# Kernel tuning notes

Hardware: AMD Instinct MI355X
Metric: run time of the kernel (lower is better)

The kernel has to match this reference:

```python
import jax, jax.numpy as jnp
import numpy as np
import math

B, T, D_MODEL, N_HEADS, K_CONV = 2, 2048, 2048, 16, 4
HEAD_DIM = D_MODEL // N_HEADS
EPS_GN = 1e-5


def setup_inputs() -> dict:
    key = jax.random.key(0)
    ks = jax.random.split(key, 16)
    s = 0.02
    # gamma bias init per reset_parameters (decays 0.9..0.9999 per head)
    min_d, max_d = 0.9, 0.9999
    tgt = 1.0 - np.exp(np.linspace(math.log(1 - min_d), math.log(1 - max_d), N_HEADS))
    gamma_bias = np.log(tgt / (1 - tgt)).astype(np.float32)
    return {
        "x": jax.random.normal(ks[0], (B, T, D_MODEL), jnp.float32),
        "Wq": jax.random.normal(ks[1], (D_MODEL, D_MODEL), jnp.float32) * s,
        "Wk": jax.random.normal(ks[2], (D_MODEL, D_MODEL), jnp.float32) * s,
        "Wv": jax.random.normal(ks[3], (D_MODEL, D_MODEL), jnp.float32) * s,
        "Wo": jax.random.normal(ks[4], (D_MODEL, D_MODEL), jnp.float32) * s,
        "conv_w": jax.random.normal(ks[5], (D_MODEL, K_CONV), jnp.float32) * 0.1,
        "conv_b": jnp.zeros((D_MODEL,), jnp.float32),
        "Wig": jax.random.normal(ks[6], (D_MODEL, D_MODEL), jnp.float32) * s,
        "b_ig": jnp.zeros((D_MODEL,), jnp.float32),
        "Wog": jax.random.normal(ks[7], (D_MODEL, D_MODEL), jnp.float32) * s,
        "b_og": jnp.zeros((D_MODEL,), jnp.float32),
        "Wg": jnp.zeros((N_HEADS, D_MODEL), jnp.float32),
        "b_g": jnp.asarray(gamma_bias),
        "gn_w": jnp.ones((D_MODEL,), jnp.float32),
        "gn_b": jnp.zeros((D_MODEL,), jnp.float32),
        "mn_w": jnp.ones((D_MODEL,), jnp.float32),
        "mn_b": jnp.zeros((D_MODEL,), jnp.float32),
    }


def _group_norm(x2d, w, b, groups, eps):
    # x2d: [N, C], normalize per group of C//groups channels
    N, C = x2d.shape
    xg = x2d.reshape(N, groups, C // groups)
    mu = xg.mean(-1, keepdims=True)
    var = ((xg - mu) ** 2).mean(-1, keepdims=True)
    xn = ((xg - mu) * jax.lax.rsqrt(var + eps)).reshape(N, C)
    return xn * w + b


def _causal_depthwise_conv(x, w, b):
    # x: [B,T,C], w: [C,K], b: [C] -> [B,T,C] causal depthwise conv + silu
    xt = jnp.transpose(x, (0, 2, 1))  # [B,C,T]
    xp = jnp.pad(xt, ((0, 0), (0, 0), (K_CONV - 1, 0)))
    y = jax.lax.conv_general_dilated(
        xp, w[:, None, :], (1,), "VALID",
        feature_group_count=D_MODEL,
        dimension_numbers=("NCH", "OIH", "NCH"))
    y = y + b[None, :, None]
    return jax.nn.silu(jnp.transpose(y, (0, 2, 1)))


def _l2norm(t):
    n = jnp.sqrt(jnp.sum(t * t, axis=-1, keepdims=True))
    return t / jnp.maximum(n, 1e-12)


def reference(x, Wq, Wk, Wv, Wo, conv_w, conv_b, Wig, b_ig, Wog, b_og, Wg, b_g, gn_w, gn_b, mn_w, mn_b):
    Bq, Tq, C = x.shape
    x_conv = _causal_depthwise_conv(x, conv_w, conv_b)  # [B,T,C]

    q = _l2norm((x @ Wq.T).reshape(Bq, Tq, N_HEADS, HEAD_DIM))
    k = _l2norm((x @ Wk.T).reshape(Bq, Tq, N_HEADS, HEAD_DIM))
    v = (x @ Wv.T).reshape(Bq, Tq, N_HEADS, HEAD_DIM)

    input_gate = jax.nn.sigmoid(x_conv @ Wig.T + b_ig).reshape(Bq, Tq, N_HEADS, HEAD_DIM)
    gamma = jax.nn.sigmoid(x_conv @ Wg.T + b_g).reshape(Bq, Tq, N_HEADS, 1)

    # gated elementwise linear recurrence: h_t = gamma_t * h_{t-1} + i_t * (k_t * v_t)
    bterm = input_gate * k * v                       # [B,T,H,D]
    aterm = jnp.broadcast_to(gamma, bterm.shape)     # [B,T,H,D]

    def scan_op(c1, c2):
        a1, b1 = c1
        a2, b2 = c2
        return (a1 * a2, a2 * b1 + b2)

    _, mem = jax.lax.associative_scan(scan_op, (aterm, bterm), axis=1)
    next_rnn_state = mem[:, -1]

    mem_n = _group_norm(mem.reshape(Bq * Tq, D_MODEL), mn_w, mn_b, N_HEADS, EPS_GN)
    mem_n = mem_n.reshape(Bq, Tq, N_HEADS, HEAD_DIM)

    out = (mem_n * q).reshape(Bq * Tq, C)
    out = _group_norm(out, gn_w, gn_b, N_HEADS, EPS_GN).reshape(Bq, Tq, C)

    output_gate = jax.nn.sigmoid(x_conv @ Wog.T + b_og)
    out = (out * output_gate) @ Wo.T

    new_conv_cache = jnp.transpose(x, (0, 2, 1))[:, :, -(K_CONV - 1):]
    return out, next_rnn_state, new_conv_cache
```

## Files before the change

kernel.cpp:

```cpp
#include <hip/hip_runtime.h>
#include <math.h>

#define B_ 2
#define T_ 2048
#define D_ 2048
#define H_ 16
#define M_ 4096
#define TD_ (T_ * D_)
#define EPS_ 1e-5f
#define NC_ 32
#define CL_ 64

typedef __bf16 bf16x8 __attribute__((ext_vector_type(8)));
typedef float f32x4 __attribute__((ext_vector_type(4)));

__device__ __forceinline__ float sigm(float z) { return 1.f / (1.f + __expf(-z)); }

__device__ __forceinline__ ushort f2bf(float f) {
    union { float f; uint u; } x; x.f = f;
    uint r = x.u + 0x7fffu + ((x.u >> 16) & 1u);
    return (ushort)(r >> 16);
}
__device__ __forceinline__ float bflo(uint u) { union { uint u; float f; } x; x.u = u << 16; return x.f; }
__device__ __forceinline__ float bfhi(uint u) { union { uint u; float f; } x; x.u = u & 0xffff0000u; return x.f; }

__device__ __forceinline__ void gload_lds16(const void* g, void* l) {
    __builtin_amdgcn_global_load_lds((const __attribute__((address_space(1))) void*)g,
                                     (__attribute__((address_space(3))) void*)l, 16, 0, 0);
}

template <int IMM>
__device__ __forceinline__ bf16x8 dsr(uint addr) {
    int4 d;
    asm volatile("ds_read_b128 %0, %1 offset:%2" : "=v"(d) : "v"(addr), "n"(IMM));
    return __builtin_bit_cast(bf16x8, d);
}
#define SCB   __builtin_amdgcn_sched_barrier(0)
#define SBAR  __builtin_amdgcn_s_barrier()

__global__ __launch_bounds__(256) void cvtw_kernel(
    const float* __restrict__ Wq, const float* __restrict__ Wk, const float* __restrict__ Wv,
    const float* __restrict__ Wig, const float* __restrict__ Wog, const float* __restrict__ Wo,
    ushort* __restrict__ W6)
{
    const int z = blockIdx.y;
    const float* src = z == 0 ? Wq : z == 1 ? Wk : z == 2 ? Wv : z == 3 ? Wig : z == 4 ? Wog : Wo;
    const int i4 = (blockIdx.x * 256 + threadIdx.x) * 4;
    float4 f = *(const float4*)(src + i4);
    ushort4 o; o.x = f2bf(f.x); o.y = f2bf(f.y); o.z = f2bf(f.z); o.w = f2bf(f.w);
    *(ushort4*)(W6 + (size_t)z * ((size_t)D_ * D_) + i4) = o;
}

__global__ __launch_bounds__(256) void conv_kernel(
    const float* __restrict__ x, const float* __restrict__ cw, const float* __restrict__ cb,
    ushort* __restrict__ xb, ushort* __restrict__ xcb, float* __restrict__ cach)
{
    const int idx = blockIdx.x * 256 + threadIdx.x;
    const int c = idx & (D_ - 1);
    const int t = (idx >> 11) & (T_ - 1);
    const int b = idx >> 22;
    const float* w = cw + c * 4;
    const float x3 = x[idx];
    float a = cb[c] + w[3] * x3;
    if (t >= 1) a += w[2] * x[idx - D_];
    if (t >= 2) a += w[1] * x[idx - 2 * D_];
    if (t >= 3) a += w[0] * x[idx - 3 * D_];
    xb[idx] = f2bf(x3);
    xcb[idx] = f2bf(a * sigm(a));
    if (t >= T_ - 3) cach[((size_t)b * D_ + c) * 3 + (t - (T_ - 3))] = x3;
}

template <bool BF16OUT>
__device__ __forceinline__ void gemm256_body(
    const ushort* __restrict__ A, const ushort* __restrict__ Bw,
    ushort* __restrict__ Cb, float* __restrict__ Cf, int bx, int by)
{
    extern __shared__ char smem[];
    const int tid = threadIdx.x;
    const int lane = tid & 63, wid = tid >> 6;
    const int wm = wid >> 1, wn = wid & 1;
    const int l15 = lane & 15, l4 = lane >> 4;
    const int brow = by * 256, bcol = bx * 128;

    const int srow = tid >> 3;
    const int scol = ((tid & 7) * 8) ^ (((tid >> 3) & 7) << 3);
    const uint sldso = (uint)tid * 16;

    f32x4 acc[4][4] = {};

    #define STAGE6(bufo, k0)                                                         \
        do {                                                                         \
            _Pragma("unroll")                                                        \
            for (int j = 0; j < 4; ++j)                                              \
                gload_lds16(A + (size_t)(brow + j * 64 + srow) * D_ + ((k0) + scol), \
                            smem + (bufo) + j * 8192 + sldso);                       \
            _Pragma("unroll")                                                        \
            for (int j = 0; j < 2; ++j)                                              \
                gload_lds16(Bw + (size_t)(bcol + j * 64 + srow) * D_ + ((k0) + scol),\
                            smem + (bufo) + 32768u + j * 8192 + sldso);              \
        } while (0)

    STAGE6(0u, 0);
    STAGE6(49152u, 64);
    asm volatile("s_waitcnt vmcnt(6)" ::: "memory");
    SBAR; SCB;

    const uint r7  = (uint)((l15 & 7) << 4);
    const uint ca0 = (uint)(l4 * 16) ^ r7;
    const uint ca1 = (uint)(64 + l4 * 16) ^ r7;
    const uint arow = (uint)(wm * 64 + l15) * 128u;
    const uint brw  = 32768u + (uint)(wn * 64 + l15) * 128u;
    const uint ldsbase = (uint)(size_t)smem;

    #pragma unroll 2
    for (int t = 0; t < 32; ++t) {
        const uint bo = ldsbase + (uint)(t & 1) * 49152u;
        const uint ab0 = bo + arow + ca0, ab1 = bo + arow + ca1;
        const uint bb0 = bo + brw + ca0,  bb1 = bo + brw + ca1;
        bf16x8 a0[8], b0[4], b1[4];
        a0[0] = dsr<0>(ab0);        a0[1] = dsr<0>(ab1);
        a0[2] = dsr<2048>(ab0);     a0[3] = dsr<2048>(ab1);
        a0[4] = dsr<4096>(ab0);     a0[5] = dsr<4096>(ab1);
        a0[6] = dsr<6144>(ab0);     a0[7] = dsr<6144>(ab1);
        b0[0] = dsr<0>(bb0);        b0[1] = dsr<0>(bb1);
        b0[2] = dsr<2048>(bb0);     b0[3] = dsr<2048>(bb1);
        b1[0] = dsr<4096>(bb0);     b1[1] = dsr<4096>(bb1);
        b1[2] = dsr<6144>(bb0);     b1[3] = dsr<6144>(bb1);
        asm volatile("s_waitcnt lgkmcnt(4)" ::: "memory");
        SCB;
        __builtin_amdgcn_s_setprio(1);
        #pragma unroll
        for (int ks = 0; ks < 2; ++ks)
            #pragma unroll
            for (int m = 0; m < 4; ++m)
                #pragma unroll
                for (int n = 0; n < 2; ++n)
                    acc[m][n] = __builtin_amdgcn_mfma_f32_16x16x32_bf16(
                        a0[m * 2 + ks], b0[n * 2 + ks], acc[m][n], 0, 0, 0);
        SCB;
        __builtin_amdgcn_s_setprio(0);
        asm volatile("s_waitcnt lgkmcnt(0)" ::: "memory");
        SCB;
        __builtin_amdgcn_s_setprio(1);
        #pragma unroll
        for (int ks = 0; ks < 2; ++ks)
            #pragma unroll
            for (int m = 0; m < 4; ++m)
                #pragma unroll
                for (int n = 0; n < 2; ++n)
                    acc[m][2 + n] = __builtin_amdgcn_mfma_f32_16x16x32_bf16(
                        a0[m * 2 + ks], b1[n * 2 + ks], acc[m][2 + n], 0, 0, 0);
        SCB;
        __builtin_amdgcn_s_setprio(0);
        if (t <= 29) {
            const uint bo2 = (uint)(t & 1) * 49152u;
            STAGE6(bo2, (t + 2) * 64);
        }
        if (t < 31) {
            if (t < 30) asm volatile("s_waitcnt vmcnt(6)" ::: "memory");
            else        asm volatile("s_waitcnt vmcnt(0)" ::: "memory");
            SBAR; SCB;
        }
    }
    #undef STAGE6

    #pragma unroll
    for (int m = 0; m < 4; ++m)
        #pragma unroll
        for (int n = 0; n < 4; ++n) {
            const int row = brow + wm * 64 + m * 16 + l4 * 4;
            const int col = bcol + wn * 64 + n * 16 + l15;
            #pragma unroll
            for (int r = 0; r < 4; ++r) {
                if (BF16OUT) Cb[(size_t)(row + r) * D_ + col] = f2bf(acc[m][n][r]);
                else         Cf[(size_t)(row + r) * D_ + col] = acc[m][n][r];
            }
        }
}

__global__ __launch_bounds__(512, 2) void gemm5_kernel(
    const ushort* __restrict__ xb, const ushort* __restrict__ xcb,
    const ushort* __restrict__ W6, ushort* __restrict__ Obuf)
{
    const int g = (blockIdx.z * 16 + blockIdx.y) * 16 + blockIdx.x;
    const int ns = (g & 7) * 160 + (g >> 3);
    const int z = ns >> 8, rem = ns & 255, by = rem >> 4, bx = rem & 15;
    const ushort* Aop = (z < 3) ? xb : xcb;
    gemm256_body<true>(Aop, W6 + (size_t)z * ((size_t)D_ * D_),
                       Obuf + (size_t)z * ((size_t)M_ * D_), nullptr, bx, by);
}

__global__ __launch_bounds__(512, 2) void gemm_out_kernel(
    const ushort* __restrict__ gated, const ushort* __restrict__ W6, float* __restrict__ out)
{
    const int g = blockIdx.y * 16 + blockIdx.x;
    const int ns = (g & 7) * 32 + (g >> 3);
    const int by = ns >> 4, bx = ns & 15;
    gemm256_body<false>(gated, W6 + (size_t)5 * ((size_t)D_ * D_), nullptr, out, bx, by);
}

__global__ __launch_bounds__(256) void gamma_kernel(
    const ushort* __restrict__ xcb, const float* __restrict__ Wg,
    const float* __restrict__ bg, float* __restrict__ gamma)
{
    __shared__ ushort xs[8 * D_];
    const int tid = threadIdx.x;
    const int tok0 = blockIdx.x * 8;
    const uint4* gsrc = (const uint4*)(xcb + (size_t)tok0 * D_);
    #pragma unroll
    for (int j = 0; j < 8; ++j)
        ((uint4*)xs)[j * 256 + tid] = gsrc[j * 256 + tid];
    __syncthreads();
    const int tok = tid >> 5;
    const int h = (tid >> 1) & 15;
    const int half = tid & 1;
    const ushort* xr = xs + tok * D_ + half * 1024;
    const float* wr = Wg + (size_t)h * D_ + half * 1024;
    float acc = 0.f;
    #pragma unroll 4
    for (int i = 0; i < 1024; i += 8) {
        uint4 u = *(const uint4*)(xr + i);
        float4 w0 = *(const float4*)(wr + i);
        float4 w1 = *(const float4*)(wr + i + 4);
        acc += bflo(u.x) * w0.x + bfhi(u.x) * w0.y + bflo(u.y) * w0.z + bfhi(u.y) * w0.w;
        acc += bflo(u.z) * w1.x + bfhi(u.z) * w1.y + bflo(u.w) * w1.z + bfhi(u.w) * w1.w;
    }
    acc += __shfl_xor(acc, 1);
    if (!half) gamma[(size_t)(tok0 + tok) * H_ + h] = sigm(acc + bg[h]);
}

__global__ __launch_bounds__(256) void bterm_kernel(
    const ushort* __restrict__ kb, const ushort* __restrict__ vb,
    const ushort* __restrict__ igb, const float* __restrict__ big,
    float* __restrict__ bt)
{
    const int token = blockIdx.x;
    const int tid = threadIdx.x;
    const int c0 = tid * 8;
    const size_t base = (size_t)token * D_ + c0;
    uint4 ku = *(const uint4*)(kb + base);
    uint4 vu = *(const uint4*)(vb + base);
    uint4 iu = *(const uint4*)(igb + base);
    float kf[8] = { bflo(ku.x), bfhi(ku.x), bflo(ku.y), bfhi(ku.y),
                    bflo(ku.z), bfhi(ku.z), bflo(ku.w), bfhi(ku.w) };
    float vf[8] = { bflo(vu.x), bfhi(vu.x), bflo(vu.y), bfhi(vu.y),
                    bflo(vu.z), bfhi(vu.z), bflo(vu.w), bfhi(vu.w) };
    float gf[8] = { bflo(iu.x), bfhi(iu.x), bflo(iu.y), bfhi(iu.y),
                    bflo(iu.z), bfhi(iu.z), bflo(iu.w), bfhi(iu.w) };
    float ss = 0.f;
    #pragma unroll
    for (int j = 0; j < 8; ++j) ss += kf[j] * kf[j];
    #pragma unroll
    for (int o = 1; o < 16; o <<= 1) ss += __shfl_xor(ss, o);
    const float sc = 1.f / fmaxf(sqrtf(ss), 1e-12f);
    float ot[8];
    #pragma unroll
    for (int j = 0; j < 8; ++j)
        ot[j] = sigm(gf[j] + big[c0 + j]) * (kf[j] * sc) * vf[j];
    float4 o0 = { ot[0], ot[1], ot[2], ot[3] };
    float4 o1 = { ot[4], ot[5], ot[6], ot[7] };
    *(float4*)(bt + base) = o0;
    *(float4*)(bt + base + 4) = o1;
}

__global__ __launch_bounds__(256) void scan1_kernel(
    const float* __restrict__ bt, const float* __restrict__ gam,
    float* __restrict__ Ab, float* __restrict__ Sb)
{
    const int c = blockIdx.x * 256 + threadIdx.x;
    const int ch = blockIdx.y, b = blockIdx.z;
    const int h = c >> 7;
    const float* g = gam + ((size_t)b * T_ + ch * CL_) * H_ + h;
    const float* p = bt + ((size_t)b * T_ + ch * CL_) * D_ + c;
    float a = 1.f, s = 0.f;
    #pragma unroll 8
    for (int i = 0; i < CL_; ++i) {
        const float gv = g[(size_t)i * H_];
        s = fmaf(gv, s, p[(size_t)i * D_]);
        a *= gv;
    }
    const size_t o = ((size_t)b * NC_ + ch) * D_ + c;
    Ab[o] = a; Sb[o] = s;
}

__global__ __launch_bounds__(256) void scan2_kernel(
    const float* __restrict__ Ab, const float* __restrict__ Sb, float* __restrict__ carry)
{
    const int idx = blockIdx.x * 256 + threadIdx.x;
    const int b = idx >> 11, c = idx & (D_ - 1);
    float run = 0.f;
    #pragma unroll
    for (int ch = 0; ch < NC_; ++ch) {
        const size_t o = ((size_t)b * NC_ + ch) * D_ + c;
        carry[o] = run;
        run = fmaf(Ab[o], run, Sb[o]);
    }
}

__global__ __launch_bounds__(256) void scan3_kernel(
    float* __restrict__ bt, const float* __restrict__ gam, const float* __restrict__ carry)
{
    const int c = blockIdx.x * 256 + threadIdx.x;
    const int ch = blockIdx.y, b = blockIdx.z;
    const int h = c >> 7;
    const float* g = gam + ((size_t)b * T_ + ch * CL_) * H_ + h;
    float* p = bt + ((size_t)b * T_ + ch * CL_) * D_ + c;
    float m = carry[((size_t)b * NC_ + ch) * D_ + c];
    #pragma unroll 8
    for (int i = 0; i < CL_; ++i) {
        m = fmaf(g[(size_t)i * H_], m, p[(size_t)i * D_]);
        p[(size_t)i * D_] = m;
    }
}

__global__ __launch_bounds__(256) void norm_kernel(
    const float* __restrict__ mem, const ushort* __restrict__ qb,
    const ushort* __restrict__ ogb, const float* __restrict__ bog,
    const float* __restrict__ mnw, const float* __restrict__ mnb,
    const float* __restrict__ gnw, const float* __restrict__ gnb,
    ushort* __restrict__ gated, float* __restrict__ rnn)
{
    const int token = blockIdx.x;
    const int tid = threadIdx.x;
    const int c0 = tid * 8;
    const size_t base = (size_t)token * D_ + c0;
    float mm[8];
    { float4 a = *(const float4*)(mem + base); float4 b2 = *(const float4*)(mem + base + 4);
      mm[0]=a.x; mm[1]=a.y; mm[2]=a.z; mm[3]=a.w; mm[4]=b2.x; mm[5]=b2.y; mm[6]=b2.z; mm[7]=b2.w; }
    float s1 = 0.f, s2 = 0.f;
    #pragma unroll
    for (int j = 0; j < 8; ++j) { s1 += mm[j]; s2 += mm[j] * mm[j]; }
    #pragma unroll
    for (int o = 1; o < 16; o <<= 1) { s1 += __shfl_xor(s1, o); s2 += __shfl_xor(s2, o); }
    const float mu = s1 * (1.f / 128.f);
    const float inv = 1.f / sqrtf(fmaxf(s2 * (1.f / 128.f) - mu * mu, 0.f) + EPS_);
    uint4 qu = *(const uint4*)(qb + base);
    float qf[8] = { bflo(qu.x), bfhi(qu.x), bflo(qu.y), bfhi(qu.y),
                    bflo(qu.z), bfhi(qu.z), bflo(qu.w), bfhi(qu.w) };
    float qs = 0.f;
    #pragma unroll
    for (int j = 0; j < 8; ++j) qs += qf[j] * qf[j];
    #pragma unroll
    for (int o = 1; o < 16; o <<= 1) qs += __shfl_xor(qs, o);
    const float qsc = 1.f / fmaxf(sqrtf(qs), 1e-12f);
    float ov[8]; float t1 = 0.f, t2 = 0.f;
    #pragma unroll
    for (int j = 0; j < 8; ++j) {
        const float mn = (mm[j] - mu) * inv * mnw[c0 + j] + mnb[c0 + j];
        ov[j] = mn * (qf[j] * qsc);
        t1 += ov[j]; t2 += ov[j] * ov[j];
    }
    #pragma unroll
    for (int o = 1; o < 16; o <<= 1) { t1 += __shfl_xor(t1, o); t2 += __shfl_xor(t2, o); }
    const float mu2 = t1 * (1.f / 128.f);
    const float inv2 = 1.f / sqrtf(fmaxf(t2 * (1.f / 128.f) - mu2 * mu2, 0.f) + EPS_);
    uint4 ou = *(const uint4*)(ogb + base);
    float of[8] = { bflo(ou.x), bfhi(ou.x), bflo(ou.y), bfhi(ou.y),
                    bflo(ou.z), bfhi(ou.z), bflo(ou.w), bfhi(ou.w) };
    uint pk[4];
    #pragma unroll
    for (int j2 = 0; j2 < 4; ++j2) {
        const int e0 = 2 * j2, e1 = 2 * j2 + 1;
        float g0 = ((ov[e0] - mu2) * inv2 * gnw[c0 + e0] + gnb[c0 + e0]) * sigm(of[e0] + bog[c0 + e0]);
        float g1 = ((ov[e1] - mu2) * inv2 * gnw[c0 + e1] + gnb[c0 + e1]) * sigm(of[e1] + bog[c0 + e1]);
        pk[j2] = (uint)f2bf(g0) | ((uint)f2bf(g1) << 16);
    }
    uint4 st = { pk[0], pk[1], pk[2], pk[3] };
    *(uint4*)(gated + base) = st;
    if ((token & (T_ - 1)) == T_ - 1) {
        float* r = rnn + (size_t)(token >> 11) * D_ + c0;
        float4 r0 = { mm[0], mm[1], mm[2], mm[3] };
        float4 r1 = { mm[4], mm[5], mm[6], mm[7] };
        *(float4*)r = r0; *(float4*)(r + 4) = r1;
    }
}

extern "C" void kernel_launch(void* const* d_in, const int* in_sizes, int n_in,
                              void* d_out, int out_size, void* d_ws, size_t ws_size,
                              hipStream_t stream)
{
    const float* x   = (const float*)d_in[0];
    const float* Wq  = (const float*)d_in[1];
    const float* Wk  = (const float*)d_in[2];
    const float* Wv  = (const float*)d_in[3];
    const float* Wo  = (const float*)d_in[4];
    const float* cw  = (const float*)d_in[5];
    const float* cb  = (const float*)d_in[6];
    const float* Wig = (const float*)d_in[7];
    const float* big = (const float*)d_in[8];
    const float* Wog = (const float*)d_in[9];
    const float* bog = (const float*)d_in[10];
    const float* Wg  = (const float*)d_in[11];
    const float* bg  = (const float*)d_in[12];
    const float* gnw = (const float*)d_in[13];
    const float* gnb = (const float*)d_in[14];
    const float* mnw = (const float*)d_in[15];
    const float* mnb = (const float*)d_in[16];

    char* ws = (char*)d_ws;
    ushort* W6   = (ushort*)ws;
    ushort* xb   = (ushort*)(ws + 50331648);
    ushort* xcb  = (ushort*)(ws + 50331648 + 16777216);
    ushort* Obuf = (ushort*)(ws + 50331648 + 2 * 16777216);
    float*  gam  = (float*)(ws + 50331648 + 7 * 16777216);
    float*  bt   = (float*)(ws + 50331648 + 7 * 16777216 + 262144);

    ushort* q    = Obuf;
    ushort* k    = Obuf + (size_t)M_ * D_;
    ushort* v    = Obuf + 2 * (size_t)M_ * D_;
    ushort* igp  = Obuf + 3 * (size_t)M_ * D_;
    ushort* ogp  = Obuf + 4 * (size_t)M_ * D_;
    ushort* gated = k;
    float*  Ab   = (float*)v;
    float*  Sb   = Ab + (size_t)B_ * NC_ * D_;
    float*  carry= Sb + (size_t)B_ * NC_ * D_;

    float* out  = (float*)d_out;
    float* rnn  = out + (size_t)M_ * D_;
    float* cach = rnn + B_ * D_;

    (void)hipFuncSetAttribute((const void*)gemm5_kernel,
                              hipFuncAttributeMaxDynamicSharedMemorySize, 98304);
    (void)hipFuncSetAttribute((const void*)gemm_out_kernel,
                              hipFuncAttributeMaxDynamicSharedMemorySize, 98304);

    cvtw_kernel<<<dim3(4096, 6), 256, 0, stream>>>(Wq, Wk, Wv, Wig, Wog, Wo, W6);
    conv_kernel<<<dim3(M_ * D_ / 256), 256, 0, stream>>>(x, cw, cb, xb, xcb, cach);
    gemm5_kernel<<<dim3(16, 16, 5), 512, 98304, stream>>>(xb, xcb, W6, Obuf);
    gamma_kernel<<<dim3(M_ / 8), 256, 0, stream>>>(xcb, Wg, bg, gam);
    bterm_kernel<<<dim3(M_), 256, 0, stream>>>(k, v, igp, big, bt);
    scan1_kernel<<<dim3(8, NC_, 2), 256, 0, stream>>>(bt, gam, Ab, Sb);
    scan2_kernel<<<dim3(16), 256, 0, stream>>>(Ab, Sb, carry);
    scan3_kernel<<<dim3(8, NC_, 2), 256, 0, stream>>>(bt, gam, carry);
    norm_kernel<<<dim3(M_), 256, 0, stream>>>(bt, q, ogp, bog, mnw, mnb, gnw, gnb, gated, rnn);
    gemm_out_kernel<<<dim3(16, 16), 512, 98304, stream>>>(gated, W6, out);
}
```

Baseline: 385.6 us.

## Fuse bterm, chunked scan passes and group norms into two scan kernels

The separate bterm, scan1, scan3 and norm kernels are replaced by scanA and scanB. Each processes one head per 64-thread wavefront over a chunk of tokens and recomputes the k-normalised gated bterm on the fly, so the fp32 bterm and mem intermediates are never written to or read from memory. scanB also applies both group norms and the output gate per token using wavefront shuffles. The chunk count goes from 32 to 64 to keep enough blocks. The cost is that k, v and input-gate loads are read twice, memory accesses become 4-byte per lane, and each step of the serial loop carries several reductions, giving 2048 small blocks with lower memory-level parallelism.

```diff
diff --git a/kernel.cpp b/kernel.cpp
--- a/kernel.cpp
+++ b/kernel.cpp
@@ -8,8 +8,8 @@
 #define M_ 4096
 #define TD_ (T_ * D_)
 #define EPS_ 1e-5f
-#define NC_ 32
-#define CL_ 64
+#define NC_ 64
+#define CL_ 32
 
 typedef __bf16 bf16x8 __attribute__((ext_vector_type(8)));
 typedef float f32x4 __attribute__((ext_vector_type(4)));
@@ -229,58 +229,37 @@
     if (!half) gamma[(size_t)(tok0 + tok) * H_ + h] = sigm(acc + bg[h]);
 }
 
-__global__ __launch_bounds__(256) void bterm_kernel(
+__global__ __launch_bounds__(64) void scanA_kernel(
     const ushort* __restrict__ kb, const ushort* __restrict__ vb,
     const ushort* __restrict__ igb, const float* __restrict__ big,
-    float* __restrict__ bt)
-{
-    const int token = blockIdx.x;
-    const int tid = threadIdx.x;
-    const int c0 = tid * 8;
-    const size_t base = (size_t)token * D_ + c0;
-    uint4 ku = *(const uint4*)(kb + base);
-    uint4 vu = *(const uint4*)(vb + base);
-    uint4 iu = *(const uint4*)(igb + base);
-    float kf[8] = { bflo(ku.x), bfhi(ku.x), bflo(ku.y), bfhi(ku.y),
-                    bflo(ku.z), bfhi(ku.z), bflo(ku.w), bfhi(ku.w) };
-    float vf[8] = { bflo(vu.x), bfhi(vu.x), bflo(vu.y), bfhi(vu.y),
-                    bflo(vu.z), bfhi(vu.z), bflo(vu.w), bfhi(vu.w) };
-    float gf[8] = { bflo(iu.x), bfhi(iu.x), bflo(iu.y), bfhi(iu.y),
-                    bflo(iu.z), bfhi(iu.z), bflo(iu.w), bfhi(iu.w) };
-    float ss = 0.f;
-    #pragma unroll
-    for (int j = 0; j < 8; ++j) ss += kf[j] * kf[j];
-    #pragma unroll
-    for (int o = 1; o < 16; o <<= 1) ss += __shfl_xor(ss, o);
-    const float sc = 1.f / fmaxf(sqrtf(ss), 1e-12f);
-    float ot[8];
-    #pragma unroll
-    for (int j = 0; j < 8; ++j)
-        ot[j] = sigm(gf[j] + big[c0 + j]) * (kf[j] * sc) * vf[j];
-    float4 o0 = { ot[0], ot[1], ot[2], ot[3] };
-    float4 o1 = { ot[4], ot[5], ot[6], ot[7] };
-    *(float4*)(bt + base) = o0;
-    *(float4*)(bt + base + 4) = o1;
-}
-
-__global__ __launch_bounds__(256) void scan1_kernel(
-    const float* __restrict__ bt, const float* __restrict__ gam,
-    float* __restrict__ Ab, float* __restrict__ Sb)
-{
-    const int c = blockIdx.x * 256 + threadIdx.x;
-    const int ch = blockIdx.y, b = blockIdx.z;
-    const int h = c >> 7;
+    const float* __restrict__ gam, float* __restrict__ Ab, float* __restrict__ Sb)
+{
+    const int l = threadIdx.x;
+    const int ch = blockIdx.x, h = blockIdx.y, b = blockIdx.z;
+    const int c0 = h * 128 + 2 * l;
+    const float bg0 = big[c0], bg1 = big[c0 + 1];
     const float* g = gam + ((size_t)b * T_ + ch * CL_) * H_ + h;
-    const float* p = bt + ((size_t)b * T_ + ch * CL_) * D_ + c;
-    float a = 1.f, s = 0.f;
-    #pragma unroll 8
+    const size_t base0 = ((size_t)b * T_ + ch * CL_) * D_ + c0;
+    float a = 1.f, sA = 0.f, sB = 0.f;
     for (int i = 0; i < CL_; ++i) {
+        const size_t off = base0 + (size_t)i * D_;
+        const uint ku = *(const uint*)(kb + off);
+        const uint vu = *(const uint*)(vb + off);
+        const uint iu = *(const uint*)(igb + off);
+        const float k0 = bflo(ku), k1 = bfhi(ku);
+        float ssq = k0 * k0 + k1 * k1;
+        #pragma unroll
+        for (int o = 1; o < 64; o <<= 1) ssq += __shfl_xor(ssq, o);
+        const float sc = 1.f / fmaxf(sqrtf(ssq), 1e-12f);
+        const float b0 = sigm(bflo(iu) + bg0) * (k0 * sc) * bflo(vu);
+        const float b1 = sigm(bfhi(iu) + bg1) * (k1 * sc) * bfhi(vu);
         const float gv = g[(size_t)i * H_];
-        s = fmaf(gv, s, p[(size_t)i * D_]);
+        sA = fmaf(gv, sA, b0);
+        sB = fmaf(gv, sB, b1);
         a *= gv;
     }
-    const size_t o = ((size_t)b * NC_ + ch) * D_ + c;
-    Ab[o] = a; Sb[o] = s;
+    const size_t o = ((size_t)b * NC_ + ch) * D_ + c0;
+    Ab[o] = a; Ab[o + 1] = a; Sb[o] = sA; Sb[o + 1] = sB;
 }
 
 __global__ __launch_bounds__(256) void scan2_kernel(
@@ -289,7 +268,7 @@
     const int idx = blockIdx.x * 256 + threadIdx.x;
     const int b = idx >> 11, c = idx & (D_ - 1);
     float run = 0.f;
-    #pragma unroll
+    #pragma unroll 8
     for (int ch = 0; ch < NC_; ++ch) {
         const size_t o = ((size_t)b * NC_ + ch) * D_ + c;
         carry[o] = run;
@@ -297,81 +276,67 @@
     }
 }
 
-__global__ __launch_bounds__(256) void scan3_kernel(
-    float* __restrict__ bt, const float* __restrict__ gam, const float* __restrict__ carry)
-{
-    const int c = blockIdx.x * 256 + threadIdx.x;
-    const int ch = blockIdx.y, b = blockIdx.z;
-    const int h = c >> 7;
+__global__ __launch_bounds__(64) void scanB_kernel(
+    const ushort* __restrict__ kb, const ushort* __restrict__ vb,
+    const ushort* __restrict__ igb, const ushort* __restrict__ qb,
+    const ushort* __restrict__ ogb, const float* __restrict__ big,
+    const float* __restrict__ bog, const float* __restrict__ mnw,
+    const float* __restrict__ mnb, const float* __restrict__ gnw,
+    const float* __restrict__ gnb, const float* __restrict__ gam,
+    const float* __restrict__ carry, ushort* __restrict__ gated,
+    float* __restrict__ rnn)
+{
+    const int l = threadIdx.x;
+    const int ch = blockIdx.x, h = blockIdx.y, b = blockIdx.z;
+    const int c0 = h * 128 + 2 * l;
+    const float bg0 = big[c0], bg1 = big[c0 + 1];
+    const float bo0 = bog[c0], bo1 = bog[c0 + 1];
+    const float mw0 = mnw[c0], mw1 = mnw[c0 + 1], mb0 = mnb[c0], mb1 = mnb[c0 + 1];
+    const float gw0 = gnw[c0], gw1 = gnw[c0 + 1], gb0 = gnb[c0], gb1 = gnb[c0 + 1];
     const float* g = gam + ((size_t)b * T_ + ch * CL_) * H_ + h;
-    float* p = bt + ((size_t)b * T_ + ch * CL_) * D_ + c;
-    float m = carry[((size_t)b * NC_ + ch) * D_ + c];
-    #pragma unroll 8
+    const size_t base0 = ((size_t)b * T_ + ch * CL_) * D_ + c0;
+    float m0 = carry[((size_t)b * NC_ + ch) * D_ + c0];
+    float m1 = carry[((size_t)b * NC_ + ch) * D_ + c0 + 1];
     for (int i = 0; i < CL_; ++i) {
-        m = fmaf(g[(size_t)i * H_], m, p[(size_t)i * D_]);
-        p[(size_t)i * D_] = m;
-    }
-}
-
-__global__ __launch_bounds__(256) void norm_kernel(
-    const float* __restrict__ mem, const ushort* __restrict__ qb,
-    const ushort* __restrict__ ogb, const float* __restrict__ bog,
-    const float* __restrict__ mnw, const float* __restrict__ mnb,
-    const float* __restrict__ gnw, const float* __restrict__ gnb,
-    ushort* __restrict__ gated, float* __restrict__ rnn)
-{
-    const int token = blockIdx.x;
-    const int tid = threadIdx.x;
-    const int c0 = tid * 8;
-    const size_t base = (size_t)token * D_ + c0;
-    float mm[8];
-    { float4 a = *(const float4*)(mem + base); float4 b2 = *(const float4*)(mem + base + 4);
-      mm[0]=a.x; mm[1]=a.y; mm[2]=a.z; mm[3]=a.w; mm[4]=b2.x; mm[5]=b2.y; mm[6]=b2.z; mm[7]=b2.w; }
-    float s1 = 0.f, s2 = 0.f;
-    #pragma unroll
-    for (int j = 0; j < 8; ++j) { s1 += mm[j]; s2 += mm[j] * mm[j]; }
-    #pragma unroll
-    for (int o = 1; o < 16; o <<= 1) { s1 += __shfl_xor(s1, o); s2 += __shfl_xor(s2, o); }
-    const float mu = s1 * (1.f / 128.f);
-    const float inv = 1.f / sqrtf(fmaxf(s2 * (1.f / 128.f) - mu * mu, 0.f) + EPS_);
-    uint4 qu = *(const uint4*)(qb + base);
-    float qf[8] = { bflo(qu.x), bfhi(qu.x), bflo(qu.y), bfhi(qu.y),
-                    bflo(qu.z), bfhi(qu.z), bflo(qu.w), bfhi(qu.w) };
-    float qs = 0.f;
-    #pragma unroll
-    for (int j = 0; j < 8; ++j) qs += qf[j] * qf[j];
-    #pragma unroll
-    for (int o = 1; o < 16; o <<= 1) qs += __shfl_xor(qs, o);
-    const float qsc = 1.f / fmaxf(sqrtf(qs), 1e-12f);
-    float ov[8]; float t1 = 0.f, t2 = 0.f;
-    #pragma unroll
-    for (int j = 0; j < 8; ++j) {
-        const float mn = (mm[j] - mu) * inv * mnw[c0 + j] + mnb[c0 + j];
-        ov[j] = mn * (qf[j] * qsc);
-        t1 += ov[j]; t2 += ov[j] * ov[j];
-    }
-    #pragma unroll
-    for (int o = 1; o < 16; o <<= 1) { t1 += __shfl_xor(t1, o); t2 += __shfl_xor(t2, o); }
-    const float mu2 = t1 * (1.f / 128.f);
-    const float inv2 = 1.f / sqrtf(fmaxf(t2 * (1.f / 128.f) - mu2 * mu2, 0.f) + EPS_);
-    uint4 ou = *(const uint4*)(ogb + base);
-    float of[8] = { bflo(ou.x), bfhi(ou.x), bflo(ou.y), bfhi(ou.y),
-                    bflo(ou.z), bfhi(ou.z), bflo(ou.w), bfhi(ou.w) };
-    uint pk[4];
-    #pragma unroll
-    for (int j2 = 0; j2 < 4; ++j2) {
-        const int e0 = 2 * j2, e1 = 2 * j2 + 1;
-        float g0 = ((ov[e0] - mu2) * inv2 * gnw[c0 + e0] + gnb[c0 + e0]) * sigm(of[e0] + bog[c0 + e0]);
-        float g1 = ((ov[e1] - mu2) * inv2 * gnw[c0 + e1] + gnb[c0 + e1]) * sigm(of[e1] + bog[c0 + e1]);
-        pk[j2] = (uint)f2bf(g0) | ((uint)f2bf(g1) << 16);
-    }
-    uint4 st = { pk[0], pk[1], pk[2], pk[3] };
-    *(uint4*)(gated + base) = st;
-    if ((token & (T_ - 1)) == T_ - 1) {
-        float* r = rnn + (size_t)(token >> 11) * D_ + c0;
-        float4 r0 = { mm[0], mm[1], mm[2], mm[3] };
-        float4 r1 = { mm[4], mm[5], mm[6], mm[7] };
-        *(float4*)r = r0; *(float4*)(r + 4) = r1;
+        const size_t off = base0 + (size_t)i * D_;
+        const uint ku = *(const uint*)(kb + off);
+        const uint vu = *(const uint*)(vb + off);
+        const uint iu = *(const uint*)(igb + off);
+        const uint qu = *(const uint*)(qb + off);
+        const uint ou = *(const uint*)(ogb + off);
+        const float k0 = bflo(ku), k1 = bfhi(ku);
+        float ssq = k0 * k0 + k1 * k1;
+        #pragma unroll
+        for (int o = 1; o < 64; o <<= 1) ssq += __shfl_xor(ssq, o);
+        const float sc = 1.f / fmaxf(sqrtf(ssq), 1e-12f);
+        const float bt0 = sigm(bflo(iu) + bg0) * (k0 * sc) * bflo(vu);
+        const float bt1 = sigm(bfhi(iu) + bg1) * (k1 * sc) * bfhi(vu);
+        const float gv = g[(size_t)i * H_];
+        m0 = fmaf(gv, m0, bt0);
+        m1 = fmaf(gv, m1, bt1);
+        const float q0 = bflo(qu), q1 = bfhi(qu);
+        float r1 = m0 + m1, r2 = m0 * m0 + m1 * m1, r3 = q0 * q0 + q1 * q1;
+        #pragma unroll
+        for (int o = 1; o < 64; o <<= 1) {
+            r1 += __shfl_xor(r1, o); r2 += __shfl_xor(r2, o); r3 += __shfl_xor(r3, o);
+        }
+        const float mu  = r1 * (1.f / 128.f);
+        const float inv = 1.f / sqrtf(fmaxf(r2 * (1.f / 128.f) - mu * mu, 0.f) + EPS_);
+        const float qsc = 1.f / fmaxf(sqrtf(r3), 1e-12f);
+        const float ov0 = ((m0 - mu) * inv * mw0 + mb0) * (q0 * qsc);
+        const float ov1 = ((m1 - mu) * inv * mw1 + mb1) * (q1 * qsc);
+        float t1 = ov0 + ov1, t2 = ov0 * ov0 + ov1 * ov1;
+        #pragma unroll
+        for (int o = 1; o < 64; o <<= 1) { t1 += __shfl_xor(t1, o); t2 += __shfl_xor(t2, o); }
+        const float mu2  = t1 * (1.f / 128.f);
+        const float inv2 = 1.f / sqrtf(fmaxf(t2 * (1.f / 128.f) - mu2 * mu2, 0.f) + EPS_);
+        const float g0 = ((ov0 - mu2) * inv2 * gw0 + gb0) * sigm(bflo(ou) + bo0);
+        const float g1 = ((ov1 - mu2) * inv2 * gw1 + gb1) * sigm(bfhi(ou) + bo1);
+        *(uint*)(gated + off) = (uint)f2bf(g0) | ((uint)f2bf(g1) << 16);
+    }
+    if (ch == NC_ - 1) {
+        rnn[(size_t)b * D_ + c0] = m0;
+        rnn[(size_t)b * D_ + c0 + 1] = m1;
     }
 }
 
@@ -402,18 +367,17 @@
     ushort* xb   = (ushort*)(ws + 50331648);
     ushort* xcb  = (ushort*)(ws + 50331648 + 16777216);
     ushort* Obuf = (ushort*)(ws + 50331648 + 2 * 16777216);
-    float*  gam  = (float*)(ws + 50331648 + 7 * 16777216);
-    float*  bt   = (float*)(ws + 50331648 + 7 * 16777216 + 262144);
+    float*  gam  = (float*)(ws + 167772160);
+    ushort* gated= (ushort*)(ws + 167772160 + 1048576);
+    float*  Ab   = (float*)(ws + 167772160 + 1048576 + 16777216);
+    float*  Sb   = Ab + (size_t)B_ * NC_ * D_;
+    float*  carry= Sb + (size_t)B_ * NC_ * D_;
 
     ushort* q    = Obuf;
     ushort* k    = Obuf + (size_t)M_ * D_;
     ushort* v    = Obuf + 2 * (size_t)M_ * D_;
     ushort* igp  = Obuf + 3 * (size_t)M_ * D_;
     ushort* ogp  = Obuf + 4 * (size_t)M_ * D_;
-    ushort* gated = k;
-    float*  Ab   = (float*)v;
-    float*  Sb   = Ab + (size_t)B_ * NC_ * D_;
-    float*  carry= Sb + (size_t)B_ * NC_ * D_;
 
     float* out  = (float*)d_out;
     float* rnn  = out + (size_t)M_ * D_;
@@ -428,10 +392,10 @@
     conv_kernel<<<dim3(M_ * D_ / 256), 256, 0, stream>>>(x, cw, cb, xb, xcb, cach);
     gemm5_kernel<<<dim3(16, 16, 5), 512, 98304, stream>>>(xb, xcb, W6, Obuf);
     gamma_kernel<<<dim3(M_ / 8), 256, 0, stream>>>(xcb, Wg, bg, gam);
-    bterm_kernel<<<dim3(M_), 256, 0, stream>>>(k, v, igp, big, bt);
-    scan1_kernel<<<dim3(8, NC_, 2), 256, 0, stream>>>(bt, gam, Ab, Sb);
+    scanA_kernel<<<dim3(NC_, H_, B_), 64, 0, stream>>>(k, v, igp, big, gam, Ab, Sb);
     scan2_kernel<<<dim3(16), 256, 0, stream>>>(Ab, Sb, carry);
-    scan3_kernel<<<dim3(8, NC_, 2), 256, 0, stream>>>(bt, gam, carry);
-    norm_kernel<<<dim3(M_), 256, 0, stream>>>(bt, q, ogp, bog, mnw, mnb, gnw, gnb, gated, rnn);
+    scanB_kernel<<<dim3(NC_, H_, B_), 64, 0, stream>>>(k, v, igp, q, ogp, big, bog,
+                                                       mnw, mnb, gnw, gnb, gam, carry,
+                                                       gated, rnn);
     gemm_out_kernel<<<dim3(16, 16), 512, 98304, stream>>>(gated, W6, out);
 }
```

Measured after the change: 416.3 us. 1.08x slower.

## Enlarge fused five-GEMM tile to 256x256 with 128KB double-buffered LDS

Applied to the files above, without the earlier changes.

The fused Q/K/V/input-gate/output-gate GEMM moves from 256x128 tiles to 256x256 tiles. Each wave now computes a 64x128 sub-tile with 32 accumulators, and the grid and tile-swizzle mapping are changed to match. The aim is higher arithmetic intensity per LDS load and fewer global loads of A, cutting memory traffic in the dominant GEMM. In exchange, LDS grows to 128KB per block and register pressure rises, which may limit occupancy to one block per CU and leave a 640-block grid with a worse tail.

```diff
diff --git a/kernel.cpp b/kernel.cpp
--- a/kernel.cpp
+++ b/kernel.cpp
@@ -70,10 +70,130 @@
     if (t >= T_ - 3) cach[((size_t)b * D_ + c) * 3 + (t - (T_ - 3))] = x3;
 }
 
-template <bool BF16OUT>
-__device__ __forceinline__ void gemm256_body(
+__device__ __forceinline__ void gemm_big_body(
     const ushort* __restrict__ A, const ushort* __restrict__ Bw,
-    ushort* __restrict__ Cb, float* __restrict__ Cf, int bx, int by)
+    ushort* __restrict__ Cb, int bx, int by)
+{
+    extern __shared__ char smem[];
+    const int tid = threadIdx.x;
+    const int lane = tid & 63, wid = tid >> 6;
+    const int wm = wid >> 1, wn = wid & 1;
+    const int l15 = lane & 15, l4 = lane >> 4;
+    const int brow = by * 256, bcol = bx * 256;
+
+    const int srow = tid >> 3;
+    const int scol = ((tid & 7) * 8) ^ (((tid >> 3) & 7) << 3);
+    const uint sldso = (uint)tid * 16;
+
+    f32x4 acc[4][8] = {};
+
+    #define STAGE8(bufo, k0)                                                         \
+        do {                                                                         \
+            _Pragma("unroll")                                                        \
+            for (int j = 0; j < 4; ++j)                                              \
+                gload_lds16(A + (size_t)(brow + j * 64 + srow) * D_ + ((k0) + scol), \
+                            smem + (bufo) + j * 8192 + sldso);                       \
+            _Pragma("unroll")                                                        \
+            for (int j = 0; j < 4; ++j)                                              \
+                gload_lds16(Bw + (size_t)(bcol + j * 64 + srow) * D_ + ((k0) + scol),\
+                            smem + (bufo) + 32768u + j * 8192 + sldso);              \
+        } while (0)
+
+    STAGE8(0u, 0);
+    STAGE8(65536u, 64);
+    asm volatile("s_waitcnt vmcnt(8)" ::: "memory");
+    SBAR; SCB;
+
+    const uint r7  = (uint)((l15 & 7) << 4);
+    const uint ca0 = (uint)(l4 * 16) ^ r7;
+    const uint ca1 = (uint)(64 + l4 * 16) ^ r7;
+    const uint arow = (uint)(wm * 64 + l15) * 128u;
+    const uint brw  = 32768u + (uint)(wn * 128 + l15) * 128u;
+    const uint ldsbase = (uint)(size_t)smem;
+
+    #pragma unroll 2
+    for (int t = 0; t < 32; ++t) {
+        const uint bo = ldsbase + (uint)(t & 1) * 65536u;
+        const uint ab0 = bo + arow + ca0, ab1 = bo + arow + ca1;
+        const uint bb0 = bo + brw + ca0,  bb1 = bo + brw + ca1;
+        bf16x8 a0[8], b0[8], b1[8];
+        a0[0] = dsr<0>(ab0);        a0[1] = dsr<0>(ab1);
+        a0[2] = dsr<2048>(ab0);     a0[3] = dsr<2048>(ab1);
+        a0[4] = dsr<4096>(ab0);     a0[5] = dsr<4096>(ab1);
+        a0[6] = dsr<6144>(ab0);     a0[7] = dsr<6144>(ab1);
+        b0[0] = dsr<0>(bb0);        b0[1] = dsr<0>(bb1);
+        b0[2] = dsr<2048>(bb0);     b0[3] = dsr<2048>(bb1);
+        b0[4] = dsr<4096>(bb0);     b0[5] = dsr<4096>(bb1);
+        b0[6] = dsr<6144>(bb0);     b0[7] = dsr<6144>(bb1);
+        b1[0] = dsr<8192>(bb0);     b1[1] = dsr<8192>(bb1);
+        b1[2] = dsr<10240>(bb0);    b1[3] = dsr<10240>(bb1);
+        b1[4] = dsr<12288>(bb0);    b1[5] = dsr<12288>(bb1);
+        b1[6] = dsr<14336>(bb0);    b1[7] = dsr<14336>(bb1);
+        asm volatile("s_waitcnt lgkmcnt(8)" ::: "memory");
+        SCB;
+        __builtin_amdgcn_s_setprio(1);
+        #pragma unroll
+        for (int ks = 0; ks < 2; ++ks)
+            #pragma unroll
+            for (int m = 0; m < 4; ++m)
+                #pragma unroll
+                for (int n = 0; n < 4; ++n)
+                    acc[m][n] = __builtin_amdgcn_mfma_f32_16x16x32_bf16(
+                        a0[m * 2 + ks], b0[n * 2 + ks], acc[m][n], 0, 0, 0);
+        SCB;
+        __builtin_amdgcn_s_setprio(0);
+        asm volatile("s_waitcnt lgkmcnt(0)" ::: "memory");
+        SCB;
+        __builtin_amdgcn_s_setprio(1);
+        #pragma unroll
+        for (int ks = 0; ks < 2; ++ks)
+            #pragma unroll
+            for (int m = 0; m < 4; ++m)
+                #pragma unroll
+                for (int n = 0; n < 4; ++n)
+                    acc[m][4 + n] = __builtin_amdgcn_mfma_f32_16x16x32_bf16(
+                        a0[m * 2 + ks], b1[n * 2 + ks], acc[m][4 + n], 0, 0, 0);
+        SCB;
+        __builtin_amdgcn_s_setprio(0);
+        if (t <= 29) {
+            const uint bo2 = (uint)(t & 1) * 65536u;
+            STAGE8(bo2, (t + 2) * 64);
+        }
+        if (t < 31) {
+            if (t < 30) asm volatile("s_waitcnt vmcnt(8)" ::: "memory");
+            else        asm volatile("s_waitcnt vmcnt(0)" ::: "memory");
+            SBAR; SCB;
+        }
+    }
+    #undef STAGE8
+
+    #pragma unroll
+    for (int m = 0; m < 4; ++m)
+        #pragma unroll
+        for (int n = 0; n < 8; ++n) {
+            const int row = brow + wm * 64 + m * 16 + l4 * 4;
+            const int col = bcol + wn * 128 + n * 16 + l15;
+            #pragma unroll
+            for (int r = 0; r < 4; ++r)
+                Cb[(size_t)(row + r) * D_ + col] = f2bf(acc[m][n][r]);
+        }
+}
+
+__global__ __launch_bounds__(512, 2) void gemm5_kernel(
+    const ushort* __restrict__ xb, const ushort* __restrict__ xcb,
+    const ushort* __restrict__ W6, ushort* __restrict__ Obuf)
+{
+    const int g = (blockIdx.z * 16 + blockIdx.y) * 8 + blockIdx.x;
+    const int ns = (g & 7) * 80 + (g >> 3);
+    const int z = ns >> 7, rem = ns & 127, by = rem >> 3, bx = rem & 7;
+    const ushort* Aop = (z < 3) ? xb : xcb;
+    gemm_big_body(Aop, W6 + (size_t)z * ((size_t)D_ * D_),
+                  Obuf + (size_t)z * ((size_t)M_ * D_), bx, by);
+}
+
+__device__ __forceinline__ void gemm_small_body(
+    const ushort* __restrict__ A, const ushort* __restrict__ Bw,
+    float* __restrict__ Cf, int bx, int by)
 {
     extern __shared__ char smem[];
     const int tid = threadIdx.x;
@@ -171,23 +291,9 @@
             const int row = brow + wm * 64 + m * 16 + l4 * 4;
             const int col = bcol + wn * 64 + n * 16 + l15;
             #pragma unroll
-            for (int r = 0; r < 4; ++r) {
-                if (BF16OUT) Cb[(size_t)(row + r) * D_ + col] = f2bf(acc[m][n][r]);
-                else         Cf[(size_t)(row + r) * D_ + col] = acc[m][n][r];
-            }
+            for (int r = 0; r < 4; ++r)
+                Cf[(size_t)(row + r) * D_ + col] = acc[m][n][r];
         }
-}
-
-__global__ __launch_bounds__(512, 2) void gemm5_kernel(
-    const ushort* __restrict__ xb, const ushort* __restrict__ xcb,
-    const ushort* __restrict__ W6, ushort* __restrict__ Obuf)
-{
-    const int g = (blockIdx.z * 16 + blockIdx.y) * 16 + blockIdx.x;
-    const int ns = (g & 7) * 160 + (g >> 3);
-    const int z = ns >> 8, rem = ns & 255, by = rem >> 4, bx = rem & 15;
-    const ushort* Aop = (z < 3) ? xb : xcb;
-    gemm256_body<true>(Aop, W6 + (size_t)z * ((size_t)D_ * D_),
-                       Obuf + (size_t)z * ((size_t)M_ * D_), nullptr, bx, by);
 }
 
 __global__ __launch_bounds__(512, 2) void gemm_out_kernel(
@@ -196,7 +302,7 @@
     const int g = blockIdx.y * 16 + blockIdx.x;
     const int ns = (g & 7) * 32 + (g >> 3);
     const int by = ns >> 4, bx = ns & 15;
-    gemm256_body<false>(gated, W6 + (size_t)5 * ((size_t)D_ * D_), nullptr, out, bx, by);
+    gemm_small_body(gated, W6 + (size_t)5 * ((size_t)D_ * D_), out, bx, by);
 }
 
 __global__ __launch_bounds__(256) void gamma_kernel(
@@ -420,13 +526,13 @@
     float* cach = rnn + B_ * D_;
 
     (void)hipFuncSetAttribute((const void*)gemm5_kernel,
-                              hipFuncAttributeMaxDynamicSharedMemorySize, 98304);
+                              hipFuncAttributeMaxDynamicSharedMemorySize, 131072);
     (void)hipFuncSetAttribute((const void*)gemm_out_kernel,
                               hipFuncAttributeMaxDynamicSharedMemorySize, 98304);
 
     cvtw_kernel<<<dim3(4096, 6), 256, 0, stream>>>(Wq, Wk, Wv, Wig, Wog, Wo, W6);
     conv_kernel<<<dim3(M_ * D_ / 256), 256, 0, stream>>>(x, cw, cb, xb, xcb, cach);
-    gemm5_kernel<<<dim3(16, 16, 5), 512, 98304, stream>>>(xb, xcb, W6, Obuf);
+    gemm5_kernel<<<dim3(8, 16, 5), 512, 131072, stream>>>(xb, xcb, W6, Obuf);
     gamma_kernel<<<dim3(M_ / 8), 256, 0, stream>>>(xcb, Wg, bg, gam);
     bterm_kernel<<<dim3(M_), 256, 0, stream>>>(k, v, igp, big, bt);
     scan1_kernel<<<dim3(8, NC_, 2), 256, 0, stream>>>(bt, gam, Ab, Sb);
```

Measured after the change: 567.5 us. 1.47x slower.
